# Kernel tuning notes

Measured on AMD Instinct MI355X. Metric: run time of the kernel, lower is better.

Reference implementation:

```python
import jax, jax.numpy as jnp
import numpy as np

N, T, INPUT_DIM, HIDDEN_DIM = 8, 4096, 128, 128


def setup_inputs() -> dict:
    key = jax.random.key(0)
    k_h, k_wq, k_bq, k_wk, k_bk = jax.random.split(key, 5)
    s = 1.0 / np.sqrt(INPUT_DIM)
    return {
        "H": jax.random.normal(k_h, (N, T, INPUT_DIM), dtype=jnp.float32),
        "Wq": jax.random.uniform(k_wq, (INPUT_DIM, HIDDEN_DIM), jnp.float32, -s, s),
        "bq": jax.random.uniform(k_bq, (HIDDEN_DIM,), jnp.float32, -s, s),
        "Wk": jax.random.uniform(k_wk, (INPUT_DIM, HIDDEN_DIM), jnp.float32, -s, s),
        "bk": jax.random.uniform(k_bk, (HIDDEN_DIM,), jnp.float32, -s, s),
    }


def reference(H, Wq, bq, Wk, bk):
    # Q, K: [N, T, hidden]
    Q = jnp.einsum("ntd,dh->nth", H, Wq) + bq
    K = jnp.einsum("ntd,dh->nth", H, Wk) + bk
    # Faithful quirk: original scales by sqrt(K.transpose(-1,-2).size(-1)) == sqrt(T),
    # NOT sqrt(hidden_dim).
    T_ = H.shape[1]
    scale = 1.0 / jnp.sqrt(jnp.asarray(T_, dtype=H.dtype))
    A = jnp.einsum("nth,nsh->nts", Q, K) * scale  # [N, T, T]
    A = jax.nn.softmax(A, axis=-1)
    # Attention applied directly to H (no V projection), plus residual.
    return jnp.einsum("nts,nsd->ntd", A, H) + H
```

## Files before the change

kernel.cpp:

```cpp
#include <hip/hip_runtime.h>
#include <hip/hip_bf16.h>

typedef __attribute__((ext_vector_type(4))) float f32x4;
typedef __attribute__((ext_vector_type(16))) float f32x16;
typedef __attribute__((ext_vector_type(8))) short s16x8;
typedef unsigned int u32;

#define DEVINL static __device__ __forceinline__

constexpr int TDIM = 4096;
constexpr int DDIM = 128;
constexpr float QSCALE = 1.4426950408889634f / 64.0f;

DEVINL unsigned short f2bf(float f) {
  union { float f; unsigned u; } v; v.f = f;
  unsigned r = v.u + 0x7fffu + ((v.u >> 16) & 1u);
  return (unsigned short)(r >> 16);
}

__global__ void wtrans_kernel(const float* __restrict__ Wq,
                              const float* __restrict__ Wk,
                              unsigned short* __restrict__ Wtq,
                              unsigned short* __restrict__ Wtk) {
  const float* src = blockIdx.x ? Wk : Wq;
  unsigned short* dst = blockIdx.x ? Wtk : Wtq;
  int tid = threadIdx.x;
  for (int k = 0; k < 64; ++k) {
    int e = tid + k * 256;
    int h = e >> 7, d = e & 127;
    dst[h * 128 + d] = f2bf(src[d * 128 + h]);
  }
}

__global__ __launch_bounds__(256) void proj_kernel(
    const float* __restrict__ H, const float* __restrict__ bq,
    const float* __restrict__ bk, const unsigned short* __restrict__ Wtq,
    const unsigned short* __restrict__ Wtk, unsigned short* __restrict__ Qb,
    char* __restrict__ Kb, char* __restrict__ Vt) {
  __shared__ __align__(16) unsigned short hs[64][136];
  int b = blockIdx.x;
  int n = b >> 6;
  int t0 = (b & 63) << 6;
  int tid = threadIdx.x;
  const float* Hrow = H + (size_t)(n * TDIM + t0) * DDIM;
#pragma unroll
  for (int k = 0; k < 8; ++k) {
    int e = tid + k * 256;
    int r = e >> 5;
    int c = (e & 31) << 2;
    f32x4 v = *(const f32x4*)(Hrow + r * DDIM + c);
    unsigned short* p = &hs[r][c];
    p[0] = f2bf(v.x); p[1] = f2bf(v.y); p[2] = f2bf(v.z); p[3] = f2bf(v.w);
  }
  __syncthreads();
  int w = tid >> 6, ln = tid & 63;
  int lm = ln & 15, lg = ln >> 4;
  int m0 = w * 16;
  s16x8 af[4];
#pragma unroll
  for (int kf = 0; kf < 4; ++kf)
    af[kf] = *(const s16x8*)&hs[m0 + lm][kf * 32 + lg * 8];
#pragma unroll
  for (int nt = 0; nt < 8; ++nt) {
    f32x4 acc = {0.f, 0.f, 0.f, 0.f};
#pragma unroll
    for (int kf = 0; kf < 4; ++kf) {
      s16x8 bfr = *(const s16x8*)&Wtq[(nt * 16 + lm) * 128 + kf * 32 + lg * 8];
      acc = __builtin_amdgcn_mfma_f32_16x16x32_bf16(af[kf], bfr, acc, 0, 0, 0);
    }
    int h = nt * 16 + lm;
    float bv = bq[h];
#pragma unroll
    for (int i = 0; i < 4; ++i) {
      int t = t0 + m0 + lg * 4 + i;
      Qb[(size_t)(n * TDIM + t) * DDIM + h] = f2bf((acc[i] + bv) * QSCALE);
    }
  }
#pragma unroll
  for (int nt = 0; nt < 8; ++nt) {
    f32x4 acc = {0.f, 0.f, 0.f, 0.f};
#pragma unroll
    for (int kf = 0; kf < 4; ++kf) {
      s16x8 bfr = *(const s16x8*)&Wtk[(nt * 16 + lm) * 128 + kf * 32 + lg * 8];
      acc = __builtin_amdgcn_mfma_f32_16x16x32_bf16(af[kf], bfr, acc, 0, 0, 0);
    }
    int h = nt * 16 + lm;
    float bv = bk[h];
#pragma unroll
    for (int i = 0; i < 4; ++i) {
      int r = m0 + lg * 4 + i;
      int lin = (r * 256 + h * 2) ^ ((r & 7) << 4);
      *(unsigned short*)(Kb + (size_t)(n * TDIM + t0) * 256 + lin) =
          f2bf(acc[i] + bv);
    }
  }
#pragma unroll
  for (int k = 0; k < 32; ++k) {
    int e = tid + k * 256;
    int d = e >> 6, tl = e & 63;
    int lin = (d * 128 + tl * 2) ^ ((d & 7) << 4);
    *(unsigned short*)(Vt + ((size_t)(n * 64 + (t0 >> 6)) << 14) + lin) =
        hs[tl][d];
  }
}

DEVINL void stage16(const char* g, char* s, int w, int ln) {
#pragma unroll
  for (int j = 0; j < 2; ++j) {
    int off = (w * 2 + j) * 1024;
    __builtin_amdgcn_global_load_lds(
        (const __attribute__((address_space(1))) void*)(g + off + ln * 16),
        (__attribute__((address_space(3))) void*)(s + off), 16, 0, 0);
  }
}

__global__ __launch_bounds__(512, 2) void attn_kernel(
    const unsigned short* __restrict__ Qb, const char* __restrict__ Ksw,
    const char* __restrict__ Vsw, const float* __restrict__ H,
    float* __restrict__ Out) {
  __shared__ __align__(16) char lds[131072];
  int b = blockIdx.x;
  int n = b & 7;
  int q0 = (b >> 3) << 7;
  int tid = threadIdx.x;
  int w = tid >> 6, ln = tid & 63;
  int q32 = ln & 31, hi = ln >> 5;
  int ws = w & 3;
  int st = w >> 2;
  int qrow = q0 + ws * 32;
  int swz = (q32 & 7) << 4;

  const char* Kn0 = Ksw + (size_t)n * (TDIM * 256);
  const char* Kn1 = Kn0 + 2048 * 256;
  const char* Vn0 = Vsw + (size_t)n * (64 * 16384);
  const char* Vn1 = Vn0 + (size_t)32 * 16384;

  const unsigned short* Qn = Qb + ((size_t)n * TDIM + qrow + q32) * DDIM;
  s16x8 qf[8];
#pragma unroll
  for (int d = 0; d < 8; ++d) qf[d] = *(const s16x8*)(Qn + d * 16 + hi * 8);

  f32x16 o[4];
#pragma unroll
  for (int dt = 0; dt < 4; ++dt) o[dt] = (f32x16)0.0f;
  float lsum = 0.f;

  stage16(Kn0, lds + 0, w, ln);
  stage16(Kn1, lds + 32768, w, ln);
  stage16(Vn0, lds + 65536, w, ln);
  stage16(Vn1, lds + 98304, w, ln);
  __syncthreads();

  for (int it = 0; it < 32; ++it) {
    int c = it & 1;
    if (it < 31) {
      int p2 = c ^ 1;
      size_t go = (size_t)(it + 1) * 16384;
      stage16(Kn0 + go, lds + p2 * 16384, w, ln);
      stage16(Kn1 + go, lds + 32768 + p2 * 16384, w, ln);
      stage16(Vn0 + go, lds + 65536 + p2 * 16384, w, ln);
      stage16(Vn1 + go, lds + 98304 + p2 * 16384, w, ln);
    }
    const char* kb = lds + st * 32768 + c * 16384;
    const char* vb = lds + 65536 + st * 32768 + c * 16384;

    f32x16 s0 = (f32x16)0.0f, s1 = (f32x16)0.0f;
    __builtin_amdgcn_s_setprio(1);
#pragma unroll
    for (int d = 0; d < 8; ++d) {
      int col = (d * 16 + hi * 8) * 2;
      s16x8 ka0 = *(const s16x8*)(kb + ((q32 * 256 + col) ^ swz));
      s16x8 ka1 = *(const s16x8*)(kb + (((q32 + 32) * 256 + col) ^ swz));
      s0 = __builtin_amdgcn_mfma_f32_32x32x16_bf16(ka0, qf[d], s0, 0, 0, 0);
      s1 = __builtin_amdgcn_mfma_f32_32x32x16_bf16(ka1, qf[d], s1, 0, 0, 0);
    }
    __builtin_amdgcn_s_setprio(0);

    f32x16 p0, p1;
#pragma unroll
    for (int r = 0; r < 16; ++r) {
      p0[r] = __builtin_amdgcn_exp2f(s0[r]);
      p1[r] = __builtin_amdgcn_exp2f(s1[r]);
    }
    float ls = 0.f;
#pragma unroll
    for (int r = 0; r < 16; ++r) ls += p0[r] + p1[r];
    lsum += ls;

    s16x8 pa[4];
#pragma unroll
    for (int kt = 0; kt < 2; ++kt) {
      u32 P2[8];
#pragma unroll
      for (int r = 0; r < 8; ++r) {
        float e0 = kt ? p1[2 * r] : p0[2 * r];
        float e1 = kt ? p1[2 * r + 1] : p0[2 * r + 1];
        asm("v_cvt_pk_bf16_f32 %0, %1, %2" : "=v"(P2[r]) : "v"(e0), "v"(e1));
      }
#pragma unroll
      for (int b2 = 0; b2 < 2; ++b2) {
        u32 a0 = P2[b2 * 4 + 0], c0 = P2[b2 * 4 + 2];
        u32 a1 = P2[b2 * 4 + 1], c1 = P2[b2 * 4 + 3];
        asm("v_permlane32_swap_b32 %0, %1" : "+v"(a0), "+v"(c0));
        asm("v_permlane32_swap_b32 %0, %1" : "+v"(a1), "+v"(c1));
        union { u32 u[4]; s16x8 v; } pk;
        pk.u[0] = a0; pk.u[1] = a1; pk.u[2] = c0; pk.u[3] = c1;
        pa[kt * 2 + b2] = pk.v;
      }
    }

    __builtin_amdgcn_s_setprio(1);
#pragma unroll
    for (int ks = 0; ks < 4; ++ks) {
      int col = (ks * 16 + hi * 8) * 2;
#pragma unroll
      for (int dt = 0; dt < 4; ++dt) {
        s16x8 vv = *(const s16x8*)(vb + (((dt * 32 + q32) * 128 + col) ^ swz));
        o[dt] = __builtin_amdgcn_mfma_f32_32x32x16_bf16(pa[ks], vv, o[dt], 0, 0, 0);
      }
    }
    __builtin_amdgcn_s_setprio(0);
    __syncthreads();
  }

  if (w >= 4) {
    char* dst = lds + (w - 4) * 16896;
#pragma unroll
    for (int dt = 0; dt < 4; ++dt)
#pragma unroll
      for (int c4 = 0; c4 < 4; ++c4) {
        f32x4 ch = {o[dt][c4 * 4 + 0], o[dt][c4 * 4 + 1],
                    o[dt][c4 * 4 + 2], o[dt][c4 * 4 + 3]};
        *(f32x4*)(dst + ((dt * 4 + c4) * 64 + ln) * 16) = ch;
      }
    *(float*)(dst + 16384 + ln * 4) = lsum;
  }
  __syncthreads();
  if (w < 4) {
    const char* src = lds + w * 16896;
#pragma unroll
    for (int dt = 0; dt < 4; ++dt)
#pragma unroll
      for (int c4 = 0; c4 < 4; ++c4) {
        f32x4 ch = *(const f32x4*)(src + ((dt * 4 + c4) * 64 + ln) * 16);
        o[dt][c4 * 4 + 0] += ch.x; o[dt][c4 * 4 + 1] += ch.y;
        o[dt][c4 * 4 + 2] += ch.z; o[dt][c4 * 4 + 3] += ch.w;
      }
    lsum += *(const float*)(src + 16384 + ln * 4);
    u32 la = __builtin_bit_cast(u32, lsum), lb = la;
    asm("v_permlane32_swap_b32 %0, %1" : "+v"(la), "+v"(lb));
    float ltot = __builtin_bit_cast(float, la) + __builtin_bit_cast(float, lb);
    float invl = 1.0f / ltot;
    if (hi == 0) *(float*)(lds + 67584 + w * 128 + q32 * 4) = invl;
  }
  __syncthreads();
  if (w < 4) {
    const float* Hn = H + (size_t)n * TDIM * DDIM;
    float* On = Out + (size_t)n * TDIM * DDIM;
    float iv[16];
#pragma unroll
    for (int r = 0; r < 16; ++r) {
      int qr = (r & 3) + 8 * (r >> 2) + 4 * hi;
      iv[r] = *(const float*)(lds + 67584 + w * 128 + qr * 4);
    }
#pragma unroll
    for (int dt = 0; dt < 4; ++dt)
#pragma unroll
      for (int r = 0; r < 16; ++r) {
        int qr = (r & 3) + 8 * (r >> 2) + 4 * hi;
        size_t idx = (size_t)(qrow + qr) * DDIM + dt * 32 + q32;
        On[idx] = o[dt][r] * iv[r] + Hn[idx];
      }
  }
}

extern "C" void kernel_launch(void* const* d_in, const int* in_sizes, int n_in,
                              void* d_out, int out_size, void* d_ws, size_t ws_size,
                              hipStream_t stream) {
  const float* H  = (const float*)d_in[0];
  const float* Wq = (const float*)d_in[1];
  const float* bq = (const float*)d_in[2];
  const float* Wk = (const float*)d_in[3];
  const float* bk = (const float*)d_in[4];
  float* Out = (float*)d_out;
  char* ws = (char*)d_ws;
  unsigned short* Wtq = (unsigned short*)(ws);
  unsigned short* Wtk = (unsigned short*)(ws + 32768);
  unsigned short* Qb  = (unsigned short*)(ws + 65536);
  char* Kb = ws + 65536 + 8388608;
  char* Vt = ws + 65536 + 2 * 8388608;

  wtrans_kernel<<<2, 256, 0, stream>>>(Wq, Wk, Wtq, Wtk);
  proj_kernel<<<512, 256, 0, stream>>>(H, bq, bk, Wtq, Wtk, Qb, Kb, Vt);
  attn_kernel<<<256, 512, 0, stream>>>(Qb, Kb, Vt, H, Out);
}
```

Before: 112.1 us.

## Stage projection outputs in LDS and switch to 16-way XOR swizzle layouts

The projection kernel now writes Q, K and the transposed H (V) tiles into shared memory first, then stores each to global memory with coalesced 16-byte writes. Before, it used scattered 2-byte global stores. The swizzle pattern widens from 8 to 16 rows, and V is laid out with paired rows of 256 bytes. The attention kernel's LDS read addressing is updated to match, which is meant to reduce bank conflicts. This adds 48KB of LDS to the projection kernel, which may lower its occupancy.

```diff
diff --git a/kernel.cpp b/kernel.cpp
--- a/kernel.cpp
+++ b/kernel.cpp
@@ -35,9 +35,12 @@
 __global__ __launch_bounds__(256) void proj_kernel(
     const float* __restrict__ H, const float* __restrict__ bq,
     const float* __restrict__ bk, const unsigned short* __restrict__ Wtq,
-    const unsigned short* __restrict__ Wtk, unsigned short* __restrict__ Qb,
+    const unsigned short* __restrict__ Wtk, char* __restrict__ Qb,
     char* __restrict__ Kb, char* __restrict__ Vt) {
   __shared__ __align__(16) unsigned short hs[64][136];
+  __shared__ __align__(16) char qs[16384];
+  __shared__ __align__(16) char kt[16384];
+  __shared__ __align__(16) char vt[16384];
   int b = blockIdx.x;
   int n = b >> 6;
   int t0 = (b & 63) << 6;
@@ -49,8 +52,16 @@
     int r = e >> 5;
     int c = (e & 31) << 2;
     f32x4 v = *(const f32x4*)(Hrow + r * DDIM + c);
+    unsigned short bf[4] = {f2bf(v.x), f2bf(v.y), f2bf(v.z), f2bf(v.w)};
     unsigned short* p = &hs[r][c];
-    p[0] = f2bf(v.x); p[1] = f2bf(v.y); p[2] = f2bf(v.z); p[3] = f2bf(v.w);
+    p[0] = bf[0]; p[1] = bf[1]; p[2] = bf[2]; p[3] = bf[3];
+#pragma unroll
+    for (int j = 0; j < 4; ++j) {
+      int d = c + j;
+      int byte = ((d >> 1) * 256 + (d & 1) * 128 + r * 2) ^
+                 (((d >> 1) & 15) << 4);
+      *(unsigned short*)(vt + byte) = bf[j];
+    }
   }
   __syncthreads();
   int w = tid >> 6, ln = tid & 63;
@@ -72,8 +83,9 @@
     float bv = bq[h];
 #pragma unroll
     for (int i = 0; i < 4; ++i) {
-      int t = t0 + m0 + lg * 4 + i;
-      Qb[(size_t)(n * TDIM + t) * DDIM + h] = f2bf((acc[i] + bv) * QSCALE);
+      int tl = m0 + lg * 4 + i;
+      int byte = tl * 256 + ((h * 2) ^ ((tl & 15) << 4));
+      *(unsigned short*)(qs + byte) = f2bf((acc[i] + bv) * QSCALE);
     }
   }
 #pragma unroll
@@ -88,19 +100,20 @@
     float bv = bk[h];
 #pragma unroll
     for (int i = 0; i < 4; ++i) {
-      int r = m0 + lg * 4 + i;
-      int lin = (r * 256 + h * 2) ^ ((r & 7) << 4);
-      *(unsigned short*)(Kb + (size_t)(n * TDIM + t0) * 256 + lin) =
-          f2bf(acc[i] + bv);
-    }
-  }
-#pragma unroll
-  for (int k = 0; k < 32; ++k) {
-    int e = tid + k * 256;
-    int d = e >> 6, tl = e & 63;
-    int lin = (d * 128 + tl * 2) ^ ((d & 7) << 4);
-    *(unsigned short*)(Vt + ((size_t)(n * 64 + (t0 >> 6)) << 14) + lin) =
-        hs[tl][d];
+      int rl = m0 + lg * 4 + i;
+      int byte = rl * 256 + ((h * 2) ^ ((rl & 15) << 4));
+      *(unsigned short*)(kt + byte) = f2bf(acc[i] + bv);
+    }
+  }
+  __syncthreads();
+  size_t base = (size_t)(n * TDIM + t0) * 256;
+  size_t vbase = ((size_t)(n * 64 + (t0 >> 6)) << 14);
+#pragma unroll
+  for (int k = 0; k < 4; ++k) {
+    int off = tid * 16 + k * 4096;
+    *(f32x4*)(Qb + base + off) = *(const f32x4*)(qs + off);
+    *(f32x4*)(Kb + base + off) = *(const f32x4*)(kt + off);
+    *(f32x4*)(Vt + vbase + off) = *(const f32x4*)(vt + off);
   }
 }
 
@@ -115,7 +128,7 @@
 }
 
 __global__ __launch_bounds__(512, 2) void attn_kernel(
-    const unsigned short* __restrict__ Qb, const char* __restrict__ Ksw,
+    const char* __restrict__ Qsw, const char* __restrict__ Ksw,
     const char* __restrict__ Vsw, const float* __restrict__ H,
     float* __restrict__ Out) {
   __shared__ __align__(16) char lds[131072];
@@ -128,17 +141,21 @@
   int ws = w & 3;
   int st = w >> 2;
   int qrow = q0 + ws * 32;
-  int swz = (q32 & 7) << 4;
+  int swz = (q32 & 15) << 4;
+  int dpl = q32 >> 1;
+  int vswz = dpl << 4;
+  int dphalf = (q32 & 1) * 128;
 
   const char* Kn0 = Ksw + (size_t)n * (TDIM * 256);
   const char* Kn1 = Kn0 + 2048 * 256;
   const char* Vn0 = Vsw + (size_t)n * (64 * 16384);
   const char* Vn1 = Vn0 + (size_t)32 * 16384;
 
-  const unsigned short* Qn = Qb + ((size_t)n * TDIM + qrow + q32) * DDIM;
+  const char* Qn = Qsw + (size_t)(n * TDIM + qrow + q32) * 256;
   s16x8 qf[8];
 #pragma unroll
-  for (int d = 0; d < 8; ++d) qf[d] = *(const s16x8*)(Qn + d * 16 + hi * 8);
+  for (int d = 0; d < 8; ++d)
+    qf[d] = *(const s16x8*)(Qn + ((d * 32 + hi * 16) ^ swz));
 
   f32x16 o[4];
 #pragma unroll
@@ -168,7 +185,7 @@
     __builtin_amdgcn_s_setprio(1);
 #pragma unroll
     for (int d = 0; d < 8; ++d) {
-      int col = (d * 16 + hi * 8) * 2;
+      int col = d * 32 + hi * 16;
       s16x8 ka0 = *(const s16x8*)(kb + ((q32 * 256 + col) ^ swz));
       s16x8 ka1 = *(const s16x8*)(kb + (((q32 + 32) * 256 + col) ^ swz));
       s0 = __builtin_amdgcn_mfma_f32_32x32x16_bf16(ka0, qf[d], s0, 0, 0, 0);
@@ -212,10 +229,11 @@
     __builtin_amdgcn_s_setprio(1);
 #pragma unroll
     for (int ks = 0; ks < 4; ++ks) {
-      int col = (ks * 16 + hi * 8) * 2;
+      int colv = dphalf + ks * 32 + hi * 16;
 #pragma unroll
       for (int dt = 0; dt < 4; ++dt) {
-        s16x8 vv = *(const s16x8*)(vb + (((dt * 32 + q32) * 128 + col) ^ swz));
+        int dp = dt * 16 + dpl;
+        s16x8 vv = *(const s16x8*)(vb + ((dp * 256 + colv) ^ vswz));
         o[dt] = __builtin_amdgcn_mfma_f32_32x32x16_bf16(pa[ks], vv, o[dt], 0, 0, 0);
       }
     }
@@ -286,7 +304,7 @@
   char* ws = (char*)d_ws;
   unsigned short* Wtq = (unsigned short*)(ws);
   unsigned short* Wtk = (unsigned short*)(ws + 32768);
-  unsigned short* Qb  = (unsigned short*)(ws + 65536);
+  char* Qb = ws + 65536;
   char* Kb = ws + 65536 + 8388608;
   char* Vt = ws + 65536 + 2 * 8388608;
 
```

Measured after the change: 108.5 us. 1.03x faster.
